# Kernel optimization log

Measured on AMD Instinct MI355X. Metric: run time of the kernel, lower is better.

The kernel has to match this reference:

```python
import jax, jax.numpy as jnp
import numpy as np

NEG = -1e6  # masked_softmax fill value from the original code


def setup_inputs() -> dict:
    key = jax.random.key(0)
    ks = jax.random.split(key, 8)
    B, Q, K, Dq, Dk, Dv, H = 8, 256, 1024, 256, 256, 128, 128
    queries = jax.random.normal(ks[0], (B, Q, Dq), dtype=jnp.float32)
    keys = jax.random.normal(ks[1], (B, K, Dk), dtype=jnp.float32)
    values = jax.random.normal(ks[2], (B, K, Dv), dtype=jnp.float32)
    valid_lens = jax.random.randint(ks[3], (B,), 1, K + 1, dtype=jnp.int32)
    # learned params (Dense, use_bias=False): y = x @ W
    W_q = jax.random.normal(ks[4], (Dq, H), dtype=jnp.float32) / np.sqrt(Dq)
    W_k = jax.random.normal(ks[5], (Dk, H), dtype=jnp.float32) / np.sqrt(Dk)
    w_v = jax.random.normal(ks[6], (H,), dtype=jnp.float32) / np.sqrt(H)
    return {"queries": queries, "keys": keys, "values": values,
            "valid_lens": valid_lens, "W_q": W_q, "W_k": W_k, "w_v": w_v}


def reference(queries, keys, values, valid_lens, W_q, W_k, w_v):
    q = jnp.einsum('bqd,dh->bqh', queries, W_q)          # [B,Q,H]
    k = jnp.einsum('bkd,dh->bkh', keys, W_k)             # [B,K,H]
    features = jnp.tanh(q[:, :, None, :] + k[:, None, :, :])  # [B,Q,K,H]
    scores = jnp.einsum('bqkh,h->bqk', features, w_v)    # [B,Q,K]
    # masked softmax over last axis: positions >= valid_len set to -1e6
    K_len = scores.shape[-1]
    mask = jnp.arange(K_len)[None, None, :] < valid_lens[:, None, None]
    scores = jnp.where(mask, scores, NEG)
    attn = jax.nn.softmax(scores, axis=-1)
    return jnp.einsum('bqk,bkv->bqv', attn, values)      # [B,Q,Dv]
```

## Files before the change

### kernel.cpp

```cpp
#include <hip/hip_runtime.h>
#include <hip/hip_bf16.h>

#if defined(__has_builtin)
#if __has_builtin(__builtin_amdgcn_exp2f)
#define EXP2F __builtin_amdgcn_exp2f
#endif
#if __has_builtin(__builtin_amdgcn_rcpf)
#define RCPF __builtin_amdgcn_rcpf
#endif
#endif
#ifndef EXP2F
#define EXP2F exp2f
#endif
#ifndef RCPF
#define RCPF(x) (1.0f / (x))
#endif

#define B_  8
#define Q_  256
#define K_  1024
#define D_  256
#define H_  128
#define DV_ 128

#define CSL 2.8853900817779268f
#define L2E 1.4426950408889634f

#define QE_OFF   0
#define KE_OFF   262144
#define WPK_OFF  1310720

__global__ __launch_bounds__(256) void proj_kernel(
    const float* __restrict__ queries, const float* __restrict__ keys,
    const float* __restrict__ Wq, const float* __restrict__ Wk,
    const float* __restrict__ w_v,
    float* __restrict__ qE, float2* __restrict__ kET2, float* __restrict__ wpk)
{
    __shared__ __align__(16) float As[64][68];
    __shared__ __align__(16) float Ws[64][128];

    const int tid = threadIdx.x;
    const int blk = blockIdx.x;
    const bool isQ = blk < 32;
    const int row0 = isQ ? blk * 64 : (blk - 32) * 64;
    const float* A = isQ ? (queries + row0 * D_) : (keys + row0 * D_);
    const float* W = isQ ? Wq : Wk;

    float acc[4][8];
#pragma unroll
    for (int i = 0; i < 4; i++)
#pragma unroll
        for (int j = 0; j < 8; j++) acc[i][j] = 0.f;

    const int lr  = tid & 63;
    const int ldb = (tid >> 6) * 16;
    const int r4  = (tid >> 4) * 4;
    const int c8  = (tid & 15) * 8;

    for (int d0 = 0; d0 < D_; d0 += 64) {
#pragma unroll
        for (int j = 0; j < 4; j++) {
            const float4 a = *(const float4*)&A[lr * D_ + d0 + ldb + j * 4];
            As[ldb + j * 4 + 0][lr] = a.x;
            As[ldb + j * 4 + 1][lr] = a.y;
            As[ldb + j * 4 + 2][lr] = a.z;
            As[ldb + j * 4 + 3][lr] = a.w;
        }
#pragma unroll
        for (int l = 0; l < 8; l++) {
            const int idx = tid + l * 256;
            const int rr = idx >> 5, cc = (idx & 31) * 4;
            *(float4*)&Ws[rr][cc] = *(const float4*)&W[(d0 + rr) * H_ + cc];
        }
        __syncthreads();
#pragma unroll 4
        for (int d = 0; d < 64; d++) {
            const float4 a4 = *(const float4*)&As[d][r4];
            const float4 w0 = *(const float4*)&Ws[d][c8];
            const float4 w1 = *(const float4*)&Ws[d][c8 + 4];
            const float ar[4] = {a4.x, a4.y, a4.z, a4.w};
#pragma unroll
            for (int i = 0; i < 4; i++) {
                acc[i][0] = fmaf(ar[i], w0.x, acc[i][0]);
                acc[i][1] = fmaf(ar[i], w0.y, acc[i][1]);
                acc[i][2] = fmaf(ar[i], w0.z, acc[i][2]);
                acc[i][3] = fmaf(ar[i], w0.w, acc[i][3]);
                acc[i][4] = fmaf(ar[i], w1.x, acc[i][4]);
                acc[i][5] = fmaf(ar[i], w1.y, acc[i][5]);
                acc[i][6] = fmaf(ar[i], w1.z, acc[i][6]);
                acc[i][7] = fmaf(ar[i], w1.w, acc[i][7]);
            }
        }
        __syncthreads();
    }

#pragma unroll
    for (int i = 0; i < 4; i++) {
        float e[8];
#pragma unroll
        for (int j = 0; j < 8; j++) e[j] = EXP2F(CSL * acc[i][j]);
        const int row = row0 + r4 + i;
        if (isQ) {
            float* dst = qE + row * H_ + c8;
            *(float4*)dst = make_float4(e[0], e[1], e[2], e[3]);
            *(float4*)(dst + 4) = make_float4(e[4], e[5], e[6], e[7]);
        } else {
            const int b = row >> 10, k = row & 1023;
            float2* dst = kET2 + (size_t)(b * 64 + (c8 >> 1)) * K_ + k;
#pragma unroll
            for (int jj = 0; jj < 4; jj++)
                dst[jj * K_] = make_float2(e[2 * jj], e[2 * jj + 1]);
        }
    }

    if (blk == 0 && tid < 64) {
        const float w1 = -2.0f * L2E * w_v[2 * tid];
        const float w2 = -2.0f * L2E * w_v[2 * tid + 1];
        *(float4*)&wpk[tid * 4] = make_float4(w1, w2, w1 + w2, 0.f);
    }
}

__global__ __launch_bounds__(1024, 8) void attn_kernel(
    const float* __restrict__ qE,
    const float2* __restrict__ kET2,
    const float* __restrict__ values,
    const int*   __restrict__ valid_lens,
    const float* __restrict__ wpk,
    float* __restrict__ out)
{
    __shared__ __align__(16) float sc[K_][4];
    __shared__ __align__(16) float red[16][4][128];
    __shared__ __align__(16) float psum[16][4];
    __shared__ float rl[4];

    const int tid = threadIdx.x;
    const int b  = blockIdx.y;
    const int q0 = blockIdx.x * 4;
    const int vl = valid_lens[b];

    const float* q0p = qE + (b * Q_ + q0) * H_;
    const float* q1p = q0p + H_;
    const float* q2p = q0p + 2 * H_;
    const float* q3p = q0p + 3 * H_;
    const float2* kb2 = kET2 + (size_t)(b * 64) * K_ + tid;

    float2 acc01 = make_float2(0.f, 0.f);
    float2 acc23 = make_float2(0.f, 0.f);

    if (tid < vl) {
#pragma unroll 4
        for (int p = 0; p < 64; p++) {
            const float2 ek = kb2[(size_t)p * K_];
            const float4 wp = *(const float4*)&wpk[p * 4];
            const float2 qa = *(const float2*)&q0p[2 * p];
            const float2 qb = *(const float2*)&q1p[2 * p];
            const float2 qc = *(const float2*)&q2p[2 * p];
            const float2 qd = *(const float2*)&q3p[2 * p];
            {
                float2 x1 = make_float2(qa.x * ek.x, qb.x * ek.x);
                float2 x2 = make_float2(qa.y * ek.y, qb.y * ek.y);
                float2 e1 = make_float2(x1.x + 1.f, x1.y + 1.f);
                float2 d  = make_float2(fmaf(e1.x, x2.x, e1.x), fmaf(e1.y, x2.y, e1.y));
                float2 n  = make_float2(fmaf(wp.y, x1.x, wp.z), fmaf(wp.y, x1.y, wp.z));
                n = make_float2(fmaf(wp.x, x2.x, n.x), fmaf(wp.x, x2.y, n.y));
                acc01.x = fmaf(n.x, RCPF(d.x), acc01.x);
                acc01.y = fmaf(n.y, RCPF(d.y), acc01.y);
            }
            {
                float2 x1 = make_float2(qc.x * ek.x, qd.x * ek.x);
                float2 x2 = make_float2(qc.y * ek.y, qd.y * ek.y);
                float2 e1 = make_float2(x1.x + 1.f, x1.y + 1.f);
                float2 d  = make_float2(fmaf(e1.x, x2.x, e1.x), fmaf(e1.y, x2.y, e1.y));
                float2 n  = make_float2(fmaf(wp.y, x1.x, wp.z), fmaf(wp.y, x1.y, wp.z));
                n = make_float2(fmaf(wp.x, x2.x, n.x), fmaf(wp.x, x2.y, n.y));
                acc23.x = fmaf(n.x, RCPF(d.x), acc23.x);
                acc23.y = fmaf(n.y, RCPF(d.y), acc23.y);
            }
        }
    }

    const bool valid = tid < vl;
    float4 pv;
    pv.x = valid ? EXP2F(acc01.x) : 0.f;
    pv.y = valid ? EXP2F(acc01.y) : 0.f;
    pv.z = valid ? EXP2F(acc23.x) : 0.f;
    pv.w = valid ? EXP2F(acc23.y) : 0.f;
    *(float4*)&sc[tid][0] = pv;

    float4 s = pv;
#pragma unroll
    for (int sh = 32; sh > 0; sh >>= 1) {
        s.x += __shfl_xor(s.x, sh);
        s.y += __shfl_xor(s.y, sh);
        s.z += __shfl_xor(s.z, sh);
        s.w += __shfl_xor(s.w, sh);
    }
    const int lane = tid & 63, w = tid >> 6;
    if (lane == 0) *(float4*)&psum[w][0] = s;
    __syncthreads();
    if (tid < 4) {
        float t = 0.f;
#pragma unroll
        for (int ww = 0; ww < 16; ww++) t += psum[ww][tid];
        rl[tid] = RCPF(t);
    }

    const int vg = (tid & 31) * 4;
    const int kh = (tid >> 5) & 1;
    const int kc = tid >> 6;
    const float* vb = values + (size_t)b * (K_ * DV_) + vg;
    float av[4][4];
#pragma unroll
    for (int q = 0; q < 4; q++)
#pragma unroll
        for (int j = 0; j < 4; j++) av[q][j] = 0.f;

    const int rem = vl - kc * 64 - kh;
    const int imax = rem <= 0 ? 0 : (((rem + 1) >> 1) > 32 ? 32 : ((rem + 1) >> 1));
#pragma unroll 2
    for (int i = 0; i < imax; i++) {
        const int k = kc * 64 + i * 2 + kh;
        const float4 vv = *(const float4*)&vb[k * DV_];
        const float4 p = *(const float4*)&sc[k][0];
        av[0][0] = fmaf(p.x, vv.x, av[0][0]); av[0][1] = fmaf(p.x, vv.y, av[0][1]);
        av[0][2] = fmaf(p.x, vv.z, av[0][2]); av[0][3] = fmaf(p.x, vv.w, av[0][3]);
        av[1][0] = fmaf(p.y, vv.x, av[1][0]); av[1][1] = fmaf(p.y, vv.y, av[1][1]);
        av[1][2] = fmaf(p.y, vv.z, av[1][2]); av[1][3] = fmaf(p.y, vv.w, av[1][3]);
        av[2][0] = fmaf(p.z, vv.x, av[2][0]); av[2][1] = fmaf(p.z, vv.y, av[2][1]);
        av[2][2] = fmaf(p.z, vv.z, av[2][2]); av[2][3] = fmaf(p.z, vv.w, av[2][3]);
        av[3][0] = fmaf(p.w, vv.x, av[3][0]); av[3][1] = fmaf(p.w, vv.y, av[3][1]);
        av[3][2] = fmaf(p.w, vv.z, av[3][2]); av[3][3] = fmaf(p.w, vv.w, av[3][3]);
    }
#pragma unroll
    for (int q = 0; q < 4; q++)
#pragma unroll
        for (int j = 0; j < 4; j++) av[q][j] += __shfl_xor(av[q][j], 32);
    if (kh == 0) {
#pragma unroll
        for (int q = 0; q < 4; q++)
            *(float4*)&red[kc][q][vg] = make_float4(av[q][0], av[q][1], av[q][2], av[q][3]);
    }
    __syncthreads();

    if (tid < 512) {
        const int q = tid >> 7, v = tid & 127;
        float t = 0.f;
#pragma unroll
        for (int g = 0; g < 16; g++) t += red[g][q][v];
        out[(b * Q_ + q0 + q) * DV_ + v] = t * rl[q];
    }
}

extern "C" void kernel_launch(void* const* d_in, const int* in_sizes, int n_in,
                              void* d_out, int out_size, void* d_ws, size_t ws_size,
                              hipStream_t stream) {
    const float* queries    = (const float*)d_in[0];
    const float* keys       = (const float*)d_in[1];
    const float* values     = (const float*)d_in[2];
    const int*   valid_lens = (const int*)d_in[3];
    const float* W_q        = (const float*)d_in[4];
    const float* W_k        = (const float*)d_in[5];
    const float* w_v        = (const float*)d_in[6];
    float* out = (float*)d_out;

    float*  ws   = (float*)d_ws;
    float*  qE   = ws + QE_OFF;
    float2* kET2 = (float2*)(ws + KE_OFF);
    float*  wpk  = ws + WPK_OFF;

    proj_kernel<<<160, 256, 0, stream>>>(queries, keys, W_q, W_k, w_v, qE, kET2, wpk);
    attn_kernel<<<dim3(Q_ / 4, B_), 1024, 0, stream>>>(qE, kET2, values, valid_lens, wpk, out);
}
```

Baseline: 120.8 us.

## Combine tanh pairs into quads to share one reciprocal, use float4 key layout

The attention scoring loop now processes four hidden units per step. Two pairwise rational tanh terms are merged over a common denominator, so each quad needs one reciprocal instead of two, and keys are loaded as float4 from a repacked layout. The projection kernel moves to 512 threads with a smaller per-thread tile and writes the new layout. The attention grid is flattened and remapped so that batches with different valid lengths are interleaved for load balance. Multiplying denominators together risks overflow or loss of precision when the exponentials are large.

```diff
diff --git a/kernel.cpp b/kernel.cpp
--- a/kernel.cpp
+++ b/kernel.cpp
@@ -30,11 +30,11 @@
 #define KE_OFF   262144
 #define WPK_OFF  1310720
 
-__global__ __launch_bounds__(256) void proj_kernel(
+__global__ __launch_bounds__(512) void proj_kernel(
     const float* __restrict__ queries, const float* __restrict__ keys,
     const float* __restrict__ Wq, const float* __restrict__ Wk,
     const float* __restrict__ w_v,
-    float* __restrict__ qE, float2* __restrict__ kET2, float* __restrict__ wpk)
+    float* __restrict__ qE, float4* __restrict__ kET4, float* __restrict__ wpk)
 {
     __shared__ __align__(16) float As[64][68];
     __shared__ __align__(16) float Ws[64][128];
@@ -46,20 +46,20 @@
     const float* A = isQ ? (queries + row0 * D_) : (keys + row0 * D_);
     const float* W = isQ ? Wq : Wk;
 
-    float acc[4][8];
-#pragma unroll
-    for (int i = 0; i < 4; i++)
+    float acc[2][8];
+#pragma unroll
+    for (int i = 0; i < 2; i++)
 #pragma unroll
         for (int j = 0; j < 8; j++) acc[i][j] = 0.f;
 
     const int lr  = tid & 63;
-    const int ldb = (tid >> 6) * 16;
-    const int r4  = (tid >> 4) * 4;
-    const int c8  = (tid & 15) * 8;
+    const int ldb = (tid >> 6) * 8;
+    const int r2  = (tid >> 4) * 2;
+    const int c4  = (tid & 15) * 4;
 
     for (int d0 = 0; d0 < D_; d0 += 64) {
 #pragma unroll
-        for (int j = 0; j < 4; j++) {
+        for (int j = 0; j < 2; j++) {
             const float4 a = *(const float4*)&A[lr * D_ + d0 + ldb + j * 4];
             As[ldb + j * 4 + 0][lr] = a.x;
             As[ldb + j * 4 + 1][lr] = a.y;
@@ -67,62 +67,69 @@
             As[ldb + j * 4 + 3][lr] = a.w;
         }
 #pragma unroll
-        for (int l = 0; l < 8; l++) {
-            const int idx = tid + l * 256;
+        for (int l = 0; l < 4; l++) {
+            const int idx = tid + l * 512;
             const int rr = idx >> 5, cc = (idx & 31) * 4;
             *(float4*)&Ws[rr][cc] = *(const float4*)&W[(d0 + rr) * H_ + cc];
         }
         __syncthreads();
 #pragma unroll 4
         for (int d = 0; d < 64; d++) {
-            const float4 a4 = *(const float4*)&As[d][r4];
-            const float4 w0 = *(const float4*)&Ws[d][c8];
-            const float4 w1 = *(const float4*)&Ws[d][c8 + 4];
-            const float ar[4] = {a4.x, a4.y, a4.z, a4.w};
-#pragma unroll
-            for (int i = 0; i < 4; i++) {
-                acc[i][0] = fmaf(ar[i], w0.x, acc[i][0]);
-                acc[i][1] = fmaf(ar[i], w0.y, acc[i][1]);
-                acc[i][2] = fmaf(ar[i], w0.z, acc[i][2]);
-                acc[i][3] = fmaf(ar[i], w0.w, acc[i][3]);
-                acc[i][4] = fmaf(ar[i], w1.x, acc[i][4]);
-                acc[i][5] = fmaf(ar[i], w1.y, acc[i][5]);
-                acc[i][6] = fmaf(ar[i], w1.z, acc[i][6]);
-                acc[i][7] = fmaf(ar[i], w1.w, acc[i][7]);
-            }
+            const float2 a2 = *(const float2*)&As[d][r2];
+            const float4 w0 = *(const float4*)&Ws[d][c4];
+            const float4 w1 = *(const float4*)&Ws[d][c4 + 64];
+            acc[0][0] = fmaf(a2.x, w0.x, acc[0][0]);
+            acc[0][1] = fmaf(a2.x, w0.y, acc[0][1]);
+            acc[0][2] = fmaf(a2.x, w0.z, acc[0][2]);
+            acc[0][3] = fmaf(a2.x, w0.w, acc[0][3]);
+            acc[0][4] = fmaf(a2.x, w1.x, acc[0][4]);
+            acc[0][5] = fmaf(a2.x, w1.y, acc[0][5]);
+            acc[0][6] = fmaf(a2.x, w1.z, acc[0][6]);
+            acc[0][7] = fmaf(a2.x, w1.w, acc[0][7]);
+            acc[1][0] = fmaf(a2.y, w0.x, acc[1][0]);
+            acc[1][1] = fmaf(a2.y, w0.y, acc[1][1]);
+            acc[1][2] = fmaf(a2.y, w0.z, acc[1][2]);
+            acc[1][3] = fmaf(a2.y, w0.w, acc[1][3]);
+            acc[1][4] = fmaf(a2.y, w1.x, acc[1][4]);
+            acc[1][5] = fmaf(a2.y, w1.y, acc[1][5]);
+            acc[1][6] = fmaf(a2.y, w1.z, acc[1][6]);
+            acc[1][7] = fmaf(a2.y, w1.w, acc[1][7]);
         }
         __syncthreads();
     }
 
 #pragma unroll
-    for (int i = 0; i < 4; i++) {
+    for (int i = 0; i < 2; i++) {
         float e[8];
 #pragma unroll
         for (int j = 0; j < 8; j++) e[j] = EXP2F(CSL * acc[i][j]);
-        const int row = row0 + r4 + i;
+        const int row = row0 + r2 + i;
         if (isQ) {
-            float* dst = qE + row * H_ + c8;
-            *(float4*)dst = make_float4(e[0], e[1], e[2], e[3]);
-            *(float4*)(dst + 4) = make_float4(e[4], e[5], e[6], e[7]);
+            float* dst = qE + row * H_;
+            *(float4*)(dst + c4)      = make_float4(e[0], e[1], e[2], e[3]);
+            *(float4*)(dst + 64 + c4) = make_float4(e[4], e[5], e[6], e[7]);
         } else {
             const int b = row >> 10, k = row & 1023;
-            float2* dst = kET2 + (size_t)(b * 64 + (c8 >> 1)) * K_ + k;
-#pragma unroll
-            for (int jj = 0; jj < 4; jj++)
-                dst[jj * K_] = make_float2(e[2 * jj], e[2 * jj + 1]);
-        }
-    }
-
-    if (blk == 0 && tid < 64) {
-        const float w1 = -2.0f * L2E * w_v[2 * tid];
-        const float w2 = -2.0f * L2E * w_v[2 * tid + 1];
-        *(float4*)&wpk[tid * 4] = make_float4(w1, w2, w1 + w2, 0.f);
+            const int g1 = c4 >> 2;
+            kET4[(size_t)(b * 32 + g1) * K_ + k]      = make_float4(e[0], e[1], e[2], e[3]);
+            kET4[(size_t)(b * 32 + 16 + g1) * K_ + k] = make_float4(e[4], e[5], e[6], e[7]);
+        }
+    }
+
+    if (blk == 0 && tid < 32) {
+        const float4 wv = *(const float4*)&w_v[tid * 4];
+        const float w1 = -2.0f * L2E * wv.x;
+        const float w2 = -2.0f * L2E * wv.y;
+        const float w3 = -2.0f * L2E * wv.z;
+        const float w4 = -2.0f * L2E * wv.w;
+        *(float4*)&wpk[tid * 8]     = make_float4(w1, w2, w1 + w2, 0.f);
+        *(float4*)&wpk[tid * 8 + 4] = make_float4(w3, w4, w3 + w4, 0.f);
     }
 }
 
 __global__ __launch_bounds__(1024, 8) void attn_kernel(
     const float* __restrict__ qE,
-    const float2* __restrict__ kET2,
+    const float4* __restrict__ kET4,
     const float* __restrict__ values,
     const int*   __restrict__ valid_lens,
     const float* __restrict__ wpk,
@@ -134,57 +141,63 @@
     __shared__ float rl[4];
 
     const int tid = threadIdx.x;
-    const int b  = blockIdx.y;
-    const int q0 = blockIdx.x * 4;
+    const int id = blockIdx.x;
+    const int x8 = id & 7;
+    const int j8 = id >> 3;
+    const int b  = (j8 & 1) ? ((x8 + 4) & 7) : x8;
+    const int qt = (j8 >> 1) | ((j8 & 1) << 5);
+    const int q0 = qt * 4;
     const int vl = valid_lens[b];
 
     const float* q0p = qE + (b * Q_ + q0) * H_;
     const float* q1p = q0p + H_;
     const float* q2p = q0p + 2 * H_;
     const float* q3p = q0p + 3 * H_;
-    const float2* kb2 = kET2 + (size_t)(b * 64) * K_ + tid;
-
-    float2 acc01 = make_float2(0.f, 0.f);
-    float2 acc23 = make_float2(0.f, 0.f);
+    const float4* kb4 = kET4 + (size_t)(b * 32) * K_ + tid;
+
+    float acc0 = 0.f, acc1 = 0.f, acc2 = 0.f, acc3 = 0.f;
 
     if (tid < vl) {
-#pragma unroll 4
-        for (int p = 0; p < 64; p++) {
-            const float2 ek = kb2[(size_t)p * K_];
-            const float4 wp = *(const float4*)&wpk[p * 4];
-            const float2 qa = *(const float2*)&q0p[2 * p];
-            const float2 qb = *(const float2*)&q1p[2 * p];
-            const float2 qc = *(const float2*)&q2p[2 * p];
-            const float2 qd = *(const float2*)&q3p[2 * p];
-            {
-                float2 x1 = make_float2(qa.x * ek.x, qb.x * ek.x);
-                float2 x2 = make_float2(qa.y * ek.y, qb.y * ek.y);
-                float2 e1 = make_float2(x1.x + 1.f, x1.y + 1.f);
-                float2 d  = make_float2(fmaf(e1.x, x2.x, e1.x), fmaf(e1.y, x2.y, e1.y));
-                float2 n  = make_float2(fmaf(wp.y, x1.x, wp.z), fmaf(wp.y, x1.y, wp.z));
-                n = make_float2(fmaf(wp.x, x2.x, n.x), fmaf(wp.x, x2.y, n.y));
-                acc01.x = fmaf(n.x, RCPF(d.x), acc01.x);
-                acc01.y = fmaf(n.y, RCPF(d.y), acc01.y);
+#pragma unroll 2
+        for (int g = 0; g < 32; g++) {
+            const float4 ek = kb4[(size_t)g * K_];
+            const float4 wa = *(const float4*)&wpk[g * 8];
+            const float4 wb = *(const float4*)&wpk[g * 8 + 4];
+            const float4 qa = *(const float4*)&q0p[4 * g];
+            const float4 qb = *(const float4*)&q1p[4 * g];
+            const float4 qc = *(const float4*)&q2p[4 * g];
+            const float4 qd = *(const float4*)&q3p[4 * g];
+#define ROW4(QV, ACC)                                                     \
+            {                                                             \
+                const float x1 = QV.x * ek.x, x2 = QV.y * ek.y;           \
+                const float x3 = QV.z * ek.z, x4 = QV.w * ek.w;           \
+                const float e1 = x1 + 1.f;                                \
+                const float d12 = fmaf(e1, x2, e1);                       \
+                const float e3 = x3 + 1.f;                                \
+                const float d34 = fmaf(e3, x4, e3);                       \
+                float n12 = fmaf(wa.y, x1, wa.z);                         \
+                n12 = fmaf(wa.x, x2, n12);                                \
+                float n34 = fmaf(wb.y, x3, wb.z);                         \
+                n34 = fmaf(wb.x, x4, n34);                                \
+                float Nn = n12 * d34;                                     \
+                Nn = fmaf(n34, d12, Nn);                                  \
+                const float Dd = d12 * d34;                               \
+                ACC = fmaf(Nn, RCPF(Dd), ACC);                            \
             }
-            {
-                float2 x1 = make_float2(qc.x * ek.x, qd.x * ek.x);
-                float2 x2 = make_float2(qc.y * ek.y, qd.y * ek.y);
-                float2 e1 = make_float2(x1.x + 1.f, x1.y + 1.f);
-                float2 d  = make_float2(fmaf(e1.x, x2.x, e1.x), fmaf(e1.y, x2.y, e1.y));
-                float2 n  = make_float2(fmaf(wp.y, x1.x, wp.z), fmaf(wp.y, x1.y, wp.z));
-                n = make_float2(fmaf(wp.x, x2.x, n.x), fmaf(wp.x, x2.y, n.y));
-                acc23.x = fmaf(n.x, RCPF(d.x), acc23.x);
-                acc23.y = fmaf(n.y, RCPF(d.y), acc23.y);
-            }
+            ROW4(qa, acc0)
+            ROW4(qb, acc1)
+            ROW4(qc, acc2)
+            ROW4(qd, acc3)
+#undef ROW4
         }
     }
 
     const bool valid = tid < vl;
     float4 pv;
-    pv.x = valid ? EXP2F(acc01.x) : 0.f;
-    pv.y = valid ? EXP2F(acc01.y) : 0.f;
-    pv.z = valid ? EXP2F(acc23.x) : 0.f;
-    pv.w = valid ? EXP2F(acc23.y) : 0.f;
+    pv.x = valid ? EXP2F(acc0) : 0.f;
+    pv.y = valid ? EXP2F(acc1) : 0.f;
+    pv.z = valid ? EXP2F(acc2) : 0.f;
+    pv.w = valid ? EXP2F(acc3) : 0.f;
     *(float4*)&sc[tid][0] = pv;
 
     float4 s = pv;
@@ -213,7 +226,7 @@
 #pragma unroll
     for (int q = 0; q < 4; q++)
 #pragma unroll
-        for (int j = 0; j < 4; j++) av[q][j] = 0.f;
+        for (int jj = 0; jj < 4; jj++) av[q][jj] = 0.f;
 
     const int rem = vl - kc * 64 - kh;
     const int imax = rem <= 0 ? 0 : (((rem + 1) >> 1) > 32 ? 32 : ((rem + 1) >> 1));
@@ -234,7 +247,7 @@
 #pragma unroll
     for (int q = 0; q < 4; q++)
 #pragma unroll
-        for (int j = 0; j < 4; j++) av[q][j] += __shfl_xor(av[q][j], 32);
+        for (int jj = 0; jj < 4; jj++) av[q][jj] += __shfl_xor(av[q][jj], 32);
     if (kh == 0) {
 #pragma unroll
         for (int q = 0; q < 4; q++)
@@ -265,9 +278,9 @@
 
     float*  ws   = (float*)d_ws;
     float*  qE   = ws + QE_OFF;
-    float2* kET2 = (float2*)(ws + KE_OFF);
+    float4* kET4 = (float4*)(ws + KE_OFF);
     float*  wpk  = ws + WPK_OFF;
 
-    proj_kernel<<<160, 256, 0, stream>>>(queries, keys, W_q, W_k, w_v, qE, kET2, wpk);
-    attn_kernel<<<dim3(Q_ / 4, B_), 1024, 0, stream>>>(qE, kET2, values, valid_lens, wpk, out);
+    proj_kernel<<<160, 512, 0, stream>>>(queries, keys, W_q, W_k, w_v, qE, kET4, wpk);
+    attn_kernel<<<512, 1024, 0, stream>>>(qE, kET4, values, valid_lens, wpk, out);
 }
```

Measured after the change: 119.7 us. About the same (-0.9%).
